# Performance work log

Measured on AMD Instinct MI355X. Metric: run time of the kernel, lower is better.

The kernel has to match this reference:

```python
import jax, jax.numpy as jnp
import numpy as np


def setup_inputs() -> dict:
    key = jax.random.key(0)
    k_x, k_b = jax.random.split(key)
    B, C, H, W = 32, 512, 32, 32
    x = jax.random.normal(k_x, (B, C, H, W), dtype=jnp.float32)
    beta = jax.random.normal(k_b, (1,), dtype=jnp.float32)
    return {"x": x, "beta": beta}


def reference(x, beta):
    B, C, H, W = x.shape
    feat = x.reshape(B, C, H * W)                       # [B, C, N]
    # channel-channel Gram matrix: [B, C, C]
    attn = jnp.einsum('bcn,bdn->bcd', feat, feat)
    # DANet-style reversed scores: rowmax - score, then softmax over last dim
    attn = jnp.max(attn, axis=-1, keepdims=True) - attn
    attn = jax.nn.softmax(attn, axis=-1)
    feat_e = jnp.einsum('bcd,bdn->bcn', attn, feat).reshape(B, C, H, W)
    return beta * feat_e + x
```

## Files before the change

kernel.cpp:

```cpp
#include <hip/hip_runtime.h>
#include <math.h>

constexpr int B = 32, C = 512, N = 1024;

typedef float f32x4 __attribute__((ext_vector_type(4)));
typedef _Float16 f16x8 __attribute__((ext_vector_type(8)));
typedef unsigned short u16x4 __attribute__((ext_vector_type(4)));

__device__ __forceinline__ unsigned short f32_to_f16u(float v) {
  union { _Float16 h; unsigned short u; } cv; cv.h = (_Float16)v; return cv.u;
}
__device__ __forceinline__ float f16u_to_f32(unsigned short u) {
  union { _Float16 h; unsigned short u; } cv; cv.u = u; return (float)cv.h;
}

__device__ __forceinline__ void glds16(const void* g, void* l) {
  __builtin_amdgcn_global_load_lds((const __attribute__((address_space(1))) void*)g,
                                   (__attribute__((address_space(3))) void*)l, 16, 0, 0);
}

__global__ __launch_bounds__(256) void convert_kernel(const float* __restrict__ x,
                                                      unsigned short* __restrict__ xf,
                                                      unsigned short* __restrict__ xfT) {
  const int b = blockIdx.z;
  const int cy = blockIdx.y * 64;
  const int nx = blockIdx.x * 64;
  const int t = threadIdx.x;
  const int r = t >> 4, c4 = (t & 15) * 4;

  __shared__ unsigned T[64][65];

#pragma unroll
  for (int rr = 0; rr < 64; rr += 16) {
    const int row = rr + r;
    const size_t gi = ((size_t)b * C + cy + row) * N + nx + c4;
    const float4 v = *(const float4*)&x[gi];
    u16x4 h;
    h[0] = f32_to_f16u(v.x); h[1] = f32_to_f16u(v.y);
    h[2] = f32_to_f16u(v.z); h[3] = f32_to_f16u(v.w);
    *(u16x4*)&xf[gi] = h;
    T[row][c4 + 0] = h[0]; T[row][c4 + 1] = h[1];
    T[row][c4 + 2] = h[2]; T[row][c4 + 3] = h[3];
  }
  __syncthreads();
#pragma unroll
  for (int rr = 0; rr < 64; rr += 16) {
    const int nrow = rr + r;
    u16x4 o;
    o[0] = (unsigned short)T[c4 + 0][nrow]; o[1] = (unsigned short)T[c4 + 1][nrow];
    o[2] = (unsigned short)T[c4 + 2][nrow]; o[3] = (unsigned short)T[c4 + 3][nrow];
    *(u16x4*)&xfT[((size_t)b * N + nx + nrow) * C + cy + c4] = o;
  }
}

__global__ __launch_bounds__(1024, 4) void gram_soft(const unsigned short* __restrict__ xf,
                                                     unsigned short* __restrict__ Af) {
  const int l = blockIdx.x;
  const int xcd = l & 7, seq = l >> 3;
  const int b = xcd + 8 * (seq >> 3);
  const int i0 = (seq & 7) * 64;

  const unsigned short* __restrict__ Fh = xf + (size_t)b * C * N;
  unsigned short* __restrict__ Ab = Af + (size_t)b * C * C;

  __shared__ __align__(16) unsigned short P[2][512 * 32];

  const int t = threadIdx.x, wave = t >> 6, lane = t & 63;
  const int wi = wave >> 3;
  const int wj = wave & 7;
  const int lrow = lane & 15, quad = lane >> 4;
  const int srow = lane >> 2;
  const int sel  = ((lane & 3) ^ ((lane >> 3) & 3)) * 8;

  f32x4 acc[2][4] = {};

#define STAGE(k0, nb)                                                     \
  {                                                                       \
    _Pragma("unroll")                                                     \
    for (int cc = 0; cc < 2; ++cc) {                                      \
      const int chunk = wave * 2 + cc;                                    \
      const int row = chunk * 16 + srow;                                  \
      glds16(Fh + (size_t)row * N + (k0) + sel, &P[nb][chunk * 512]);     \
    }                                                                     \
  }

  STAGE(0, 0);

  for (int it = 0; it < 32; ++it) {
    const int k0 = it * 32;
    __syncthreads();
    if (it + 1 < 32) STAGE(k0 + 32, (it + 1) & 1);

    const unsigned short* __restrict__ Pc = P[it & 1];
    f16x8 ah[2], bh[4];
#pragma unroll
    for (int ti = 0; ti < 2; ++ti) {
      const int r = i0 + wi * 32 + ti * 16 + lrow;
      ah[ti] = *(const f16x8*)&Pc[r * 32 + (quad ^ ((r >> 1) & 3)) * 8];
    }
#pragma unroll
    for (int tj = 0; tj < 4; ++tj) {
      const int r = wj * 64 + tj * 16 + lrow;
      bh[tj] = *(const f16x8*)&Pc[r * 32 + (quad ^ ((r >> 1) & 3)) * 8];
    }
#pragma unroll
    for (int ti = 0; ti < 2; ++ti)
#pragma unroll
      for (int tj = 0; tj < 4; ++tj)
        acc[ti][tj] = __builtin_amdgcn_mfma_f32_16x16x32_f16(ah[ti], bh[tj], acc[ti][tj], 0, 0, 0);
  }
#undef STAGE

  __syncthreads();
  float* red = (float*)&P[0][0];
  float* fin = red + 512;

  float m[8];
#pragma unroll
  for (int ti = 0; ti < 2; ++ti)
#pragma unroll
    for (int rr = 0; rr < 4; ++rr)
      m[ti * 4 + rr] = fminf(fminf(acc[ti][0][rr], acc[ti][1][rr]),
                             fminf(acc[ti][2][rr], acc[ti][3][rr]));
#pragma unroll
  for (int o = 1; o < 16; o <<= 1)
#pragma unroll
    for (int s = 0; s < 8; ++s) m[s] = fminf(m[s], __shfl_xor(m[s], o, 64));
  if (lrow == 0)
#pragma unroll
    for (int ti = 0; ti < 2; ++ti)
#pragma unroll
      for (int rr = 0; rr < 4; ++rr)
        red[wave * 32 + ti * 16 + quad * 4 + rr] = m[ti * 4 + rr];
  __syncthreads();
  if (t < 64) {
    const int wig = t >> 5, loc = t & 31;
    float v = red[(wig * 8) * 32 + loc];
#pragma unroll
    for (int j = 1; j < 8; ++j) v = fminf(v, red[(wig * 8 + j) * 32 + loc]);
    fin[t] = v;
  }
  __syncthreads();

  float sm[8];
#pragma unroll
  for (int ti = 0; ti < 2; ++ti)
#pragma unroll
    for (int rr = 0; rr < 4; ++rr) {
      const float mn = fin[wi * 32 + ti * 16 + quad * 4 + rr];
      float s = 0.f;
#pragma unroll
      for (int tj = 0; tj < 4; ++tj) {
        const float e = __expf(mn - acc[ti][tj][rr]);
        acc[ti][tj][rr] = e;
        s += e;
      }
      sm[ti * 4 + rr] = s;
    }
#pragma unroll
  for (int o = 1; o < 16; o <<= 1)
#pragma unroll
    for (int s = 0; s < 8; ++s) sm[s] += __shfl_xor(sm[s], o, 64);
  if (lrow == 0)
#pragma unroll
    for (int ti = 0; ti < 2; ++ti)
#pragma unroll
      for (int rr = 0; rr < 4; ++rr)
        red[wave * 32 + ti * 16 + quad * 4 + rr] = sm[ti * 4 + rr];
  __syncthreads();
  if (t < 64) {
    const int wig = t >> 5, loc = t & 31;
    float v = 0.f;
#pragma unroll
    for (int j = 0; j < 8; ++j) v += red[(wig * 8 + j) * 32 + loc];
    fin[t] = 1.0f / v;
  }
  __syncthreads();

#pragma unroll
  for (int ti = 0; ti < 2; ++ti)
#pragma unroll
    for (int rr = 0; rr < 4; ++rr) {
      const float inv = fin[wi * 32 + ti * 16 + quad * 4 + rr];
      const int grow = i0 + wi * 32 + ti * 16 + quad * 4 + rr;
#pragma unroll
      for (int tj = 0; tj < 4; ++tj) {
        const int gcol = wj * 64 + tj * 16 + lrow;
        Ab[(size_t)grow * C + gcol] = f32_to_f16u(acc[ti][tj][rr] * inv);
      }
    }
}

__global__ __launch_bounds__(256, 4) void av_mfma(const unsigned short* __restrict__ Af,
                                                  const unsigned short* __restrict__ xfT,
                                                  const unsigned short* __restrict__ xf,
                                                  const float* __restrict__ beta,
                                                  float* __restrict__ out) {
  const int l = blockIdx.x;
  const int xcd = l & 7, seq = l >> 3;
  const int b = xcd + 8 * (seq >> 5);
  const int tile = seq & 31;
  const int i0 = (tile >> 3) * 128;
  const int j0 = (tile & 7) * 128;

  const unsigned short* __restrict__ Ab = Af  + (size_t)b * C * C;
  const unsigned short* __restrict__ FT = xfT + (size_t)b * N * C;
  const unsigned short* __restrict__ xb = xf  + (size_t)b * C * N;
  float* __restrict__ ob = out + (size_t)b * C * N;

  __shared__ __align__(16) unsigned short SMEM[2 * 128 * 64];
  unsigned short* As = SMEM;
  unsigned short* Bs = SMEM + 128 * 64;

  const int t = threadIdx.x, wave = t >> 6, lane = t & 63;
  const int wi = wave >> 1, wj = wave & 1;
  const int lrow = lane & 15, quad = lane >> 4;
  const int srow8 = lane >> 3;
  const int sel = ((lane & 7) ^ srow8) * 8;

  f32x4 acc[4][4] = {};

  for (int k0 = 0; k0 < C; k0 += 64) {
    __syncthreads();
#pragma unroll
    for (int cc = 0; cc < 4; ++cc) {
      const int chunk = wave * 4 + cc;
      const int row = chunk * 8 + srow8;
      glds16(Ab + (size_t)(i0 + row) * C + k0 + sel, &As[chunk * 512]);
      glds16(FT + (size_t)(j0 + row) * C + k0 + sel, &Bs[chunk * 512]);
    }
    __syncthreads();

#pragma unroll
    for (int kh = 0; kh < 2; ++kh) {
      f16x8 af[4], bf[4];
#pragma unroll
      for (int ti = 0; ti < 4; ++ti) {
        const int r = wi * 64 + ti * 16 + lrow;
        af[ti] = *(const f16x8*)&As[r * 64 + ((kh * 4 + quad) ^ (r & 7)) * 8];
      }
#pragma unroll
      for (int tj = 0; tj < 4; ++tj) {
        const int r = wj * 64 + tj * 16 + lrow;
        bf[tj] = *(const f16x8*)&Bs[r * 64 + ((kh * 4 + quad) ^ (r & 7)) * 8];
      }
#pragma unroll
      for (int ti = 0; ti < 4; ++ti)
#pragma unroll
        for (int tj = 0; tj < 4; ++tj)
          acc[ti][tj] = __builtin_amdgcn_mfma_f32_16x16x32_f16(af[ti], bf[tj], acc[ti][tj], 0, 0, 0);
    }
  }

  __syncthreads();
  float* fs = (float*)SMEM + wave * 1024;
  const float bv = beta[0];
#pragma unroll
  for (int ti = 0; ti < 4; ++ti) {
#pragma unroll
    for (int tj = 0; tj < 4; ++tj)
#pragma unroll
      for (int r = 0; r < 4; ++r)
        fs[(quad * 4 + r) * 64 + tj * 16 + lrow] = acc[ti][tj][r];
    __syncthreads();
#pragma unroll
    for (int p = 0; p < 4; ++p) {
      const int f = p * 64 + lane;
      const int rr = f >> 4, cc4 = (f & 15) * 4;
      const f32x4 e = *(const f32x4*)&fs[rr * 64 + cc4];
      const int gr = i0 + wi * 64 + ti * 16 + rr;
      const int gc = j0 + wj * 64 + cc4;
      const size_t o = (size_t)gr * N + gc;
      const u16x4 xv = *(const u16x4*)&xb[o];
      f32x4 ov;
      ov[0] = fmaf(bv, e[0], f16u_to_f32(xv[0]));
      ov[1] = fmaf(bv, e[1], f16u_to_f32(xv[1]));
      ov[2] = fmaf(bv, e[2], f16u_to_f32(xv[2]));
      ov[3] = fmaf(bv, e[3], f16u_to_f32(xv[3]));
      __builtin_nontemporal_store(ov, (f32x4*)&ob[o]);
    }
    __syncthreads();
  }
}

extern "C" void kernel_launch(void* const* d_in, const int* in_sizes, int n_in,
                              void* d_out, int out_size, void* d_ws, size_t ws_size,
                              hipStream_t stream) {
  const float* x    = (const float*)d_in[0];
  const float* beta = (const float*)d_in[1];
  float* out = (float*)d_out;

  char* ws = (char*)d_ws;
  unsigned short* xf  = (unsigned short*)ws; ws += (size_t)B * C * N * 2;
  unsigned short* xfT = (unsigned short*)ws; ws += (size_t)B * N * C * 2;
  unsigned short* Af  = (unsigned short*)ws;

  convert_kernel<<<dim3(N / 64, C / 64, B), dim3(256),  0, stream>>>(x, xf, xfT);
  gram_soft     <<<dim3(256),               dim3(1024), 0, stream>>>(xf, Af);
  av_mfma       <<<dim3(1024),              dim3(256),  0, stream>>>(Af, xfT, xf, beta, out);
}
```

Measured before the change: 172.8 us.

## Fuse attention-times-features GEMM into gram/softmax kernel via LDS attention tile

Merges the softmax-attention computation and the attention-times-features product into one kernel. Each block keeps its normalized 64x512 attention tile in LDS in fp16 with a swizzle, then streams the transposed features to produce its output rows. This removes the global write and read of the attention matrix and one kernel launch. In exchange, only 256 blocks handle the second GEMM instead of 1024, and LDS use per block grows by 64 KB, which limits occupancy and parallelism in that phase.

```diff
diff --git a/kernel.cpp b/kernel.cpp
--- a/kernel.cpp
+++ b/kernel.cpp
@@ -53,17 +53,21 @@
   }
 }
 
-__global__ __launch_bounds__(1024, 4) void gram_soft(const unsigned short* __restrict__ xf,
-                                                     unsigned short* __restrict__ Af) {
+__global__ __launch_bounds__(1024, 4) void gram_soft_av(const unsigned short* __restrict__ xf,
+                                                        const unsigned short* __restrict__ xfT,
+                                                        const float* __restrict__ beta,
+                                                        float* __restrict__ out) {
   const int l = blockIdx.x;
   const int xcd = l & 7, seq = l >> 3;
   const int b = xcd + 8 * (seq >> 3);
   const int i0 = (seq & 7) * 64;
 
-  const unsigned short* __restrict__ Fh = xf + (size_t)b * C * N;
-  unsigned short* __restrict__ Ab = Af + (size_t)b * C * C;
-
-  __shared__ __align__(16) unsigned short P[2][512 * 32];
+  const unsigned short* __restrict__ Fh = xf  + (size_t)b * C * N;
+  const unsigned short* __restrict__ FT = xfT + (size_t)b * N * C;
+  float* __restrict__ ob = out + (size_t)b * C * N;
+
+  __shared__ __align__(16) unsigned short Pb[2][512 * 32];
+  __shared__ __align__(16) unsigned short Atile[64 * 512];
 
   const int t = threadIdx.x, wave = t >> 6, lane = t & 63;
   const int wi = wave >> 3;
@@ -80,7 +84,7 @@
     for (int cc = 0; cc < 2; ++cc) {                                      \
       const int chunk = wave * 2 + cc;                                    \
       const int row = chunk * 16 + srow;                                  \
-      glds16(Fh + (size_t)row * N + (k0) + sel, &P[nb][chunk * 512]);     \
+      glds16(Fh + (size_t)row * N + (k0) + sel, &Pb[nb][chunk * 512]);    \
     }                                                                     \
   }
 
@@ -91,7 +95,7 @@
     __syncthreads();
     if (it + 1 < 32) STAGE(k0 + 32, (it + 1) & 1);
 
-    const unsigned short* __restrict__ Pc = P[it & 1];
+    const unsigned short* __restrict__ Pc = Pb[it & 1];
     f16x8 ah[2], bh[4];
 #pragma unroll
     for (int ti = 0; ti < 2; ++ti) {
@@ -112,7 +116,7 @@
 #undef STAGE
 
   __syncthreads();
-  float* red = (float*)&P[0][0];
+  float* red = (float*)&Pb[0][0];
   float* fin = red + 512;
 
   float m[8];
@@ -182,104 +186,84 @@
 #pragma unroll
     for (int rr = 0; rr < 4; ++rr) {
       const float inv = fin[wi * 32 + ti * 16 + quad * 4 + rr];
-      const int grow = i0 + wi * 32 + ti * 16 + quad * 4 + rr;
+      const int rl = wi * 32 + ti * 16 + quad * 4 + rr;
 #pragma unroll
       for (int tj = 0; tj < 4; ++tj) {
         const int gcol = wj * 64 + tj * 16 + lrow;
-        Ab[(size_t)grow * C + gcol] = f32_to_f16u(acc[ti][tj][rr] * inv);
-      }
-    }
-}
-
-__global__ __launch_bounds__(256, 4) void av_mfma(const unsigned short* __restrict__ Af,
-                                                  const unsigned short* __restrict__ xfT,
-                                                  const unsigned short* __restrict__ xf,
-                                                  const float* __restrict__ beta,
-                                                  float* __restrict__ out) {
-  const int l = blockIdx.x;
-  const int xcd = l & 7, seq = l >> 3;
-  const int b = xcd + 8 * (seq >> 5);
-  const int tile = seq & 31;
-  const int i0 = (tile >> 3) * 128;
-  const int j0 = (tile & 7) * 128;
-
-  const unsigned short* __restrict__ Ab = Af  + (size_t)b * C * C;
-  const unsigned short* __restrict__ FT = xfT + (size_t)b * N * C;
-  const unsigned short* __restrict__ xb = xf  + (size_t)b * C * N;
-  float* __restrict__ ob = out + (size_t)b * C * N;
-
-  __shared__ __align__(16) unsigned short SMEM[2 * 128 * 64];
-  unsigned short* As = SMEM;
-  unsigned short* Bs = SMEM + 128 * 64;
-
-  const int t = threadIdx.x, wave = t >> 6, lane = t & 63;
-  const int wi = wave >> 1, wj = wave & 1;
-  const int lrow = lane & 15, quad = lane >> 4;
-  const int srow8 = lane >> 3;
-  const int sel = ((lane & 7) ^ srow8) * 8;
-
-  f32x4 acc[4][4] = {};
-
-  for (int k0 = 0; k0 < C; k0 += 64) {
+        Atile[rl * 512 + ((((gcol >> 3) ^ (rl & 7)) << 3) | (gcol & 7))] =
+            f32_to_f16u(acc[ti][tj][rr] * inv);
+      }
+    }
+  __syncthreads();
+
+  const float bv = beta[0];
+
+  for (int jp = 0; jp < 2; ++jp) {
+    f32x4 eacc[2][4] = {};
+#define STAGE_E(k0, nb)                                                        \
+    {                                                                          \
+      _Pragma("unroll")                                                        \
+      for (int cc = 0; cc < 2; ++cc) {                                         \
+        const int chunk = wave * 2 + cc;                                       \
+        const int row = chunk * 16 + srow;                                     \
+        glds16(FT + (size_t)(jp * 512 + row) * C + (k0) + sel,                 \
+               &Pb[nb][chunk * 512]);                                          \
+      }                                                                        \
+    }
+    STAGE_E(0, 0);
+    for (int it = 0; it < 16; ++it) {
+      const int k0 = it * 32;
+      __syncthreads();
+      if (it + 1 < 16) STAGE_E(k0 + 32, (it + 1) & 1);
+
+      const unsigned short* __restrict__ Pc = Pb[it & 1];
+      f16x8 ah[2], bh[4];
+#pragma unroll
+      for (int ti = 0; ti < 2; ++ti) {
+        const int ra = wi * 32 + ti * 16 + lrow;
+        ah[ti] = *(const f16x8*)&Atile[ra * 512 + ((((k0 >> 3) | quad) ^ (ra & 7)) << 3)];
+      }
+#pragma unroll
+      for (int tj = 0; tj < 4; ++tj) {
+        const int rb = wj * 64 + tj * 16 + lrow;
+        bh[tj] = *(const f16x8*)&Pc[rb * 32 + ((quad ^ ((rb >> 1) & 3)) << 3)];
+      }
+#pragma unroll
+      for (int ti = 0; ti < 2; ++ti)
+#pragma unroll
+        for (int tj = 0; tj < 4; ++tj)
+          eacc[ti][tj] = __builtin_amdgcn_mfma_f32_16x16x32_f16(ah[ti], bh[tj], eacc[ti][tj], 0, 0, 0);
+    }
+#undef STAGE_E
+
     __syncthreads();
-#pragma unroll
-    for (int cc = 0; cc < 4; ++cc) {
-      const int chunk = wave * 4 + cc;
-      const int row = chunk * 8 + srow8;
-      glds16(Ab + (size_t)(i0 + row) * C + k0 + sel, &As[chunk * 512]);
-      glds16(FT + (size_t)(j0 + row) * C + k0 + sel, &Bs[chunk * 512]);
-    }
-    __syncthreads();
-
-#pragma unroll
-    for (int kh = 0; kh < 2; ++kh) {
-      f16x8 af[4], bf[4];
-#pragma unroll
-      for (int ti = 0; ti < 4; ++ti) {
-        const int r = wi * 64 + ti * 16 + lrow;
-        af[ti] = *(const f16x8*)&As[r * 64 + ((kh * 4 + quad) ^ (r & 7)) * 8];
-      }
-#pragma unroll
-      for (int tj = 0; tj < 4; ++tj) {
-        const int r = wj * 64 + tj * 16 + lrow;
-        bf[tj] = *(const f16x8*)&Bs[r * 64 + ((kh * 4 + quad) ^ (r & 7)) * 8];
-      }
-#pragma unroll
-      for (int ti = 0; ti < 4; ++ti)
-#pragma unroll
-        for (int tj = 0; tj < 4; ++tj)
-          acc[ti][tj] = __builtin_amdgcn_mfma_f32_16x16x32_f16(af[ti], bf[tj], acc[ti][tj], 0, 0, 0);
-    }
-  }
-
-  __syncthreads();
-  float* fs = (float*)SMEM + wave * 1024;
-  const float bv = beta[0];
-#pragma unroll
-  for (int ti = 0; ti < 4; ++ti) {
-#pragma unroll
-    for (int tj = 0; tj < 4; ++tj)
-#pragma unroll
-      for (int r = 0; r < 4; ++r)
-        fs[(quad * 4 + r) * 64 + tj * 16 + lrow] = acc[ti][tj][r];
-    __syncthreads();
-#pragma unroll
-    for (int p = 0; p < 4; ++p) {
-      const int f = p * 64 + lane;
-      const int rr = f >> 4, cc4 = (f & 15) * 4;
-      const f32x4 e = *(const f32x4*)&fs[rr * 64 + cc4];
-      const int gr = i0 + wi * 64 + ti * 16 + rr;
-      const int gc = j0 + wj * 64 + cc4;
-      const size_t o = (size_t)gr * N + gc;
-      const u16x4 xv = *(const u16x4*)&xb[o];
-      f32x4 ov;
-      ov[0] = fmaf(bv, e[0], f16u_to_f32(xv[0]));
-      ov[1] = fmaf(bv, e[1], f16u_to_f32(xv[1]));
-      ov[2] = fmaf(bv, e[2], f16u_to_f32(xv[2]));
-      ov[3] = fmaf(bv, e[3], f16u_to_f32(xv[3]));
-      __builtin_nontemporal_store(ov, (f32x4*)&ob[o]);
-    }
-    __syncthreads();
+    float* fs = (float*)&Pb[0][0] + wave * 1024;
+#pragma unroll
+    for (int ti = 0; ti < 2; ++ti) {
+#pragma unroll
+      for (int tj = 0; tj < 4; ++tj)
+#pragma unroll
+        for (int r = 0; r < 4; ++r)
+          fs[(quad * 4 + r) * 64 + tj * 16 + lrow] = eacc[ti][tj][r];
+      __syncthreads();
+#pragma unroll
+      for (int p = 0; p < 4; ++p) {
+        const int f = p * 64 + lane;
+        const int rr2 = f >> 4, cc4 = (f & 15) * 4;
+        const f32x4 e = *(const f32x4*)&fs[rr2 * 64 + cc4];
+        const int gr = i0 + wi * 32 + ti * 16 + rr2;
+        const int gc = jp * 512 + wj * 64 + cc4;
+        const size_t o = (size_t)gr * N + gc;
+        const u16x4 xv = *(const u16x4*)&Fh[o];
+        f32x4 ov;
+        ov[0] = fmaf(bv, e[0], f16u_to_f32(xv[0]));
+        ov[1] = fmaf(bv, e[1], f16u_to_f32(xv[1]));
+        ov[2] = fmaf(bv, e[2], f16u_to_f32(xv[2]));
+        ov[3] = fmaf(bv, e[3], f16u_to_f32(xv[3]));
+        __builtin_nontemporal_store(ov, (f32x4*)&ob[o]);
+      }
+      __syncthreads();
+    }
   }
 }
 
@@ -292,10 +276,8 @@
 
   char* ws = (char*)d_ws;
   unsigned short* xf  = (unsigned short*)ws; ws += (size_t)B * C * N * 2;
-  unsigned short* xfT = (unsigned short*)ws; ws += (size_t)B * N * C * 2;
-  unsigned short* Af  = (unsigned short*)ws;
+  unsigned short* xfT = (unsigned short*)ws;
 
   convert_kernel<<<dim3(N / 64, C / 64, B), dim3(256),  0, stream>>>(x, xf, xfT);
-  gram_soft     <<<dim3(256),               dim3(1024), 0, stream>>>(xf, Af);
-  av_mfma       <<<dim3(1024),              dim3(256),  0, stream>>>(Af, xfT, xf, beta, out);
-}
+  gram_soft_av  <<<dim3(256),               dim3(1024), 0, stream>>>(xf, xfT, beta, out);
+}
```

Result: slower. 181.5 us (+5.0%).
